# Optimization experiments

Hardware: AMD Instinct MI355X
Metric: run time of the kernel (lower is better)

## Reference

```python
import jax, jax.numpy as jnp
import numpy as np

NUM_HEADS = 4

def setup_inputs() -> dict:
    key = jax.random.key(0)
    ks = jax.random.split(key, 5)
    B, H, W, C = 4, 64, 64, 256
    x = jax.random.normal(ks[0], (B, H, W, C), dtype=jnp.float32)
    w_qkv = jax.random.normal(ks[1], (C, 3 * C), dtype=jnp.float32) * (C ** -0.5)
    b_qkv = jax.random.normal(ks[2], (3 * C,), dtype=jnp.float32) * 0.02
    w_out = jax.random.normal(ks[3], (C, C), dtype=jnp.float32) * (C ** -0.5)
    b_out = jax.random.normal(ks[4], (C,), dtype=jnp.float32) * 0.02
    return {"x": x, "w_qkv": w_qkv, "b_qkv": b_qkv, "w_out": w_out, "b_out": b_out}

def reference(x, w_qkv, b_qkv, w_out, b_out):
    B, H, W, C = x.shape
    nh = NUM_HEADS
    hd = C // nh
    scale = hd ** -0.5
    N = H * W
    # qkv projection: [B, N, 3, nh, hd]
    qkv = (x.reshape(B, N, C) @ w_qkv + b_qkv).reshape(B, N, 3, nh, hd)
    q, k, v = jnp.moveaxis(qkv, 2, 0)          # each [B, N, nh, hd]
    q = jnp.swapaxes(q, 1, 2)                  # [B, nh, N, hd]
    k = jnp.swapaxes(k, 1, 2)
    v = jnp.swapaxes(v, 1, 2)
    attn = jax.nn.softmax(jnp.einsum('bhnd,bhmd->bhnm', q * scale, k), axis=-1)
    o = jnp.einsum('bhnm,bhmd->bhnd', attn, v)  # [B, nh, N, hd]
    o = jnp.swapaxes(o, 1, 2).reshape(B, H, W, C)
    return o @ w_out + b_out
```

## Files before the change

kernel.cpp:

```cpp
#include <hip/hip_runtime.h>
#include <stdint.h>

typedef unsigned short u16;
typedef __attribute__((ext_vector_type(8))) short bf16x8;
typedef __attribute__((ext_vector_type(4))) float f32x4;

#define QSCL 0.1803368801111244f

#define GLD_LDS16(g, l) __builtin_amdgcn_global_load_lds( \
    (const __attribute__((address_space(1))) void*)(g),    \
    (__attribute__((address_space(3))) void*)(l), 16, 0, 0)

__device__ __forceinline__ u16 f2bf(float f) {
    union { uint32_t i; float f; } v; v.f = f;
    uint32_t i = v.i;
    return (u16)((i + 0x7FFFu + ((i >> 16) & 1u)) >> 16);
}
__device__ __forceinline__ uint32_t fbits(float f) {
    union { float f; uint32_t i; } v; v.f = f; return v.i;
}
__device__ __forceinline__ float bits2f(uint32_t i) {
    union { uint32_t i; float f; } v; v.i = i; return v.f;
}

__global__ __launch_bounds__(256)
void transpose_kernel(const float* __restrict__ src, u16* __restrict__ dst,
                      int R, int Ctiles) {
    __shared__ u16 T[64][68];
    const int t = threadIdx.x;
    const int rt = blockIdx.x / Ctiles;
    const int ct = blockIdx.x % Ctiles;
    const int C = Ctiles << 6;

    for (int i = 0; i < 4; i++) {
        int idx = t + 256 * i;
        int row = idx >> 4;
        int col4 = (idx & 15) << 2;
        float4 d = *(const float4*)(src + (size_t)(rt * 64 + row) * C + ct * 64 + col4);
        T[col4 + 0][row] = f2bf(d.x);
        T[col4 + 1][row] = f2bf(d.y);
        T[col4 + 2][row] = f2bf(d.z);
        T[col4 + 3][row] = f2bf(d.w);
    }
    __syncthreads();
    for (int i = 0; i < 4; i++) {
        int idx = t + 256 * i;
        int row = idx >> 4;
        int col4 = (idx & 15) << 2;
        uint2 d = *(const uint2*)&T[row][col4];
        *(uint2*)(dst + (size_t)(ct * 64 + row) * R + rt * 64 + col4) = d;
    }
}

__global__ __launch_bounds__(256)
void convert_kernel(const float* __restrict__ x, u16* __restrict__ xbf) {
    size_t i = ((size_t)blockIdx.x * 256 + threadIdx.x) * 4;
    float4 d = *(const float4*)(x + i);
    u16 e[4] = {f2bf(d.x), f2bf(d.y), f2bf(d.z), f2bf(d.w)};
    *(uint2*)(xbf + i) = *(uint2*)e;
}

__global__ __launch_bounds__(256)
void gemm_qkv_old(const float* __restrict__ X, const u16* __restrict__ Wt,
                  const float* __restrict__ Bias, u16* __restrict__ QK,
                  u16* __restrict__ Vt) {
    __shared__ __align__(16) u16 As[64][40];
    __shared__ __align__(16) u16 Bts[64][40];

    const int t = threadIdx.x;
    const int lane = t & 63;
    const int wave = t >> 6;
    const int l15 = lane & 15;
    const int l4 = lane >> 4;

    const int ntile = blockIdx.x % 12;
    const int mbase = (blockIdx.x / 12) << 6;

    f32x4 acc[4];
    for (int c = 0; c < 4; c++) acc[c] = (f32x4){0.f, 0.f, 0.f, 0.f};

    for (int kc = 0; kc < 256; kc += 32) {
        __syncthreads();
        for (int i = 0; i < 2; i++) {
            int idx = t + 256 * i;
            int row = idx >> 3;
            int col4 = (idx & 7) << 2;
            float4 d = *(const float4*)(X + (size_t)(mbase + row) * 256 + kc + col4);
            u16 e[4] = {f2bf(d.x), f2bf(d.y), f2bf(d.z), f2bf(d.w)};
            *(uint2*)&As[row][col4] = *(uint2*)e;
        }
        for (int i = 0; i < 2; i++) {
            int idx = t + 256 * i;
            int row = idx >> 3;
            int col4 = (idx & 7) << 2;
            uint2 w = *(const uint2*)(Wt + (size_t)(ntile * 64 + row) * 256 + kc + col4);
            *(uint2*)&Bts[row][col4] = w;
        }
        __syncthreads();

        bf16x8 a = *(const bf16x8*)&As[wave * 16 + l15][l4 * 8];
        for (int c = 0; c < 4; c++) {
            bf16x8 b = *(const bf16x8*)&Bts[c * 16 + l15][l4 * 8];
            acc[c] = __builtin_amdgcn_mfma_f32_16x16x32_bf16(a, b, acc[c], 0, 0, 0);
        }
    }

    if (ntile < 8) {
        const float scl = (ntile < 4) ? QSCL : 1.0f;
        for (int c = 0; c < 4; c++) {
            int colc = c * 16 + l15;
            float bv = Bias[ntile * 64 + colc];
            for (int r = 0; r < 4; r++) {
                int row = mbase + wave * 16 + l4 * 4 + r;
                QK[(size_t)row * 512 + ntile * 64 + colc] = f2bf((acc[c][r] + bv) * scl);
            }
        }
    } else {
        const int h = ntile - 8;
        for (int c = 0; c < 4; c++) {
            int d = c * 16 + l15;
            float bv = Bias[512 + h * 64 + d];
            int n = mbase + wave * 16 + l4 * 4;
            int b = n >> 12;
            int nin = n & 4095;
            u16 e[4] = {f2bf(acc[c][0] + bv), f2bf(acc[c][1] + bv),
                        f2bf(acc[c][2] + bv), f2bf(acc[c][3] + bv)};
            *(uint2*)(Vt + ((size_t)(b * 4 + h) * 64 + d) * 4096 + nin) = *(uint2*)e;
        }
    }
}

__global__ __launch_bounds__(256)
void gemm_out_old(const u16* __restrict__ Wt2, const float* __restrict__ Bias,
                  float* __restrict__ IO) {
    __shared__ __align__(16) u16 As[64][264];
    __shared__ __align__(16) u16 Wts[256][40];

    const int t = threadIdx.x;
    const int lane = t & 63;
    const int wave = t >> 6;
    const int l15 = lane & 15;
    const int l4 = lane >> 4;
    const int mbase = blockIdx.x << 6;

    for (int i = 0; i < 16; i++) {
        int idx = t + 256 * i;
        int row = idx >> 6;
        int col4 = (idx & 63) << 2;
        float4 d = *(const float4*)(IO + (size_t)(mbase + row) * 256 + col4);
        u16 e[4] = {f2bf(d.x), f2bf(d.y), f2bf(d.z), f2bf(d.w)};
        *(uint2*)&As[row][col4] = *(uint2*)e;
    }

    f32x4 acc[4][4];
    for (int nt = 0; nt < 4; nt++)
        for (int c = 0; c < 4; c++) acc[nt][c] = (f32x4){0.f, 0.f, 0.f, 0.f};

    for (int kc = 0; kc < 256; kc += 32) {
        __syncthreads();
        for (int i = 0; i < 8; i++) {
            int idx = t + 256 * i;
            int row = idx >> 3;
            int col4 = (idx & 7) << 2;
            uint2 w = *(const uint2*)(Wt2 + (size_t)row * 256 + kc + col4);
            *(uint2*)&Wts[row][col4] = w;
        }
        __syncthreads();

        bf16x8 a = *(const bf16x8*)&As[wave * 16 + l15][kc + l4 * 8];
        for (int nt = 0; nt < 4; nt++)
            for (int c = 0; c < 4; c++) {
                bf16x8 b = *(const bf16x8*)&Wts[nt * 64 + c * 16 + l15][l4 * 8];
                acc[nt][c] = __builtin_amdgcn_mfma_f32_16x16x32_bf16(a, b, acc[nt][c], 0, 0, 0);
            }
    }

    for (int nt = 0; nt < 4; nt++)
        for (int c = 0; c < 4; c++) {
            int coln = nt * 64 + c * 16 + l15;
            float bv = Bias[coln];
            for (int r = 0; r < 4; r++) {
                int row = mbase + wave * 16 + l4 * 4 + r;
                IO[(size_t)row * 256 + coln] = acc[nt][c][r] + bv;
            }
        }
}

__global__ __launch_bounds__(256)
void gemm_qkv_new(const u16* __restrict__ Abf, const u16* __restrict__ Bt,
                  const float* __restrict__ Bias, u16* __restrict__ QK,
                  u16* __restrict__ Vt) {
    __shared__ __align__(16) u16 As[128 * 32];
    __shared__ __align__(16) u16 Bs[128 * 32];

    const int t = threadIdx.x;
    const int lane = t & 63;
    const int wave = t >> 6;
    const int l15 = lane & 15;
    const int l4 = lane >> 4;
    const int wm = wave >> 1, wn = wave & 1;

    const int mb = blockIdx.x / 6;
    const int nb = blockIdx.x % 6;

    const u16* gA[2]; const u16* gB[2]; int ldsoff[2];
    #pragma unroll
    for (int i = 0; i < 2; i++) {
        int chunk = i * 256 + t;
        int row = chunk >> 2;
        int sch = (chunk & 3) ^ (row & 3);
        gA[i] = Abf + (size_t)(mb * 128 + row) * 256 + sch * 8;
        gB[i] = Bt + (size_t)(nb * 128 + row) * 256 + sch * 8;
        ldsoff[i] = (i * 256 + wave * 64) * 8;
    }
    int offA[4], offB[4];
    #pragma unroll
    for (int c = 0; c < 4; c++) {
        offA[c] = (wm * 64 + c * 16 + l15) * 32 + ((l4 ^ (l15 & 3)) * 8);
        offB[c] = (wn * 64 + c * 16 + l15) * 32 + ((l4 ^ (l15 & 3)) * 8);
    }

    f32x4 acc[4][4];
    #pragma unroll
    for (int cm = 0; cm < 4; cm++)
        for (int cn = 0; cn < 4; cn++) acc[cm][cn] = (f32x4){0.f, 0.f, 0.f, 0.f};

    for (int kc = 0; kc < 256; kc += 32) {
        __syncthreads();
        #pragma unroll
        for (int i = 0; i < 2; i++) {
            GLD_LDS16(gA[i] + kc, As + ldsoff[i]);
            GLD_LDS16(gB[i] + kc, Bs + ldsoff[i]);
        }
        __syncthreads();

        bf16x8 a[4], b[4];
        #pragma unroll
        for (int c = 0; c < 4; c++) {
            a[c] = *(const bf16x8*)(As + offA[c]);
            b[c] = *(const bf16x8*)(Bs + offB[c]);
        }
        #pragma unroll
        for (int cm = 0; cm < 4; cm++)
            #pragma unroll
            for (int cn = 0; cn < 4; cn++)
                acc[cm][cn] = __builtin_amdgcn_mfma_f32_16x16x32_bf16(
                    a[cm], b[cn], acc[cm][cn], 0, 0, 0);
    }

    #pragma unroll
    for (int cn = 0; cn < 4; cn++) {
        int n = nb * 128 + wn * 64 + cn * 16 + l15;
        float bv = Bias[n];
        int slice = n >> 6;
        if (slice < 4) {
            #pragma unroll
            for (int cm = 0; cm < 4; cm++) {
                int m0 = mb * 128 + wm * 64 + cm * 16 + l4 * 4;
                for (int r = 0; r < 4; r++)
                    QK[(size_t)(m0 + r) * 512 + n] = f2bf((acc[cm][cn][r] + bv) * QSCL);
            }
        } else if (slice < 8) {
            #pragma unroll
            for (int cm = 0; cm < 4; cm++) {
                int m0 = mb * 128 + wm * 64 + cm * 16 + l4 * 4;
                for (int r = 0; r < 4; r++)
                    QK[(size_t)(m0 + r) * 512 + n] = f2bf(acc[cm][cn][r] + bv);
            }
        } else {
            int h = slice - 8;
            int d = n & 63;
            #pragma unroll
            for (int cm = 0; cm < 4; cm++) {
                int m0 = mb * 128 + wm * 64 + cm * 16 + l4 * 4;
                int b_ = m0 >> 12;
                int nin = m0 & 4095;
                u16 e[4] = {f2bf(acc[cm][cn][0] + bv), f2bf(acc[cm][cn][1] + bv),
                            f2bf(acc[cm][cn][2] + bv), f2bf(acc[cm][cn][3] + bv)};
                *(uint2*)(Vt + ((size_t)(b_ * 4 + h) * 64 + d) * 4096 + nin) = *(uint2*)e;
            }
        }
    }
}

__global__ __launch_bounds__(256)
void gemm_out_new(const u16* __restrict__ Obf, const u16* __restrict__ Wt2,
                  const float* __restrict__ Bias, float* __restrict__ out) {
    __shared__ __align__(16) u16 As[128 * 32];
    __shared__ __align__(16) u16 Bs[128 * 32];

    const int t = threadIdx.x;
    const int lane = t & 63;
    const int wave = t >> 6;
    const int l15 = lane & 15;
    const int l4 = lane >> 4;
    const int wm = wave >> 1, wn = wave & 1;

    const int mb = blockIdx.x >> 1;
    const int nb = blockIdx.x & 1;

    const u16* gA[2]; const u16* gB[2]; int ldsoff[2];
    #pragma unroll
    for (int i = 0; i < 2; i++) {
        int chunk = i * 256 + t;
        int row = chunk >> 2;
        int sch = (chunk & 3) ^ (row & 3);
        gA[i] = Obf + (size_t)(mb * 128 + row) * 256 + sch * 8;
        gB[i] = Wt2 + (size_t)(nb * 128 + row) * 256 + sch * 8;
        ldsoff[i] = (i * 256 + wave * 64) * 8;
    }
    int offA[4], offB[4];
    #pragma unroll
    for (int c = 0; c < 4; c++) {
        offA[c] = (wm * 64 + c * 16 + l15) * 32 + ((l4 ^ (l15 & 3)) * 8);
        offB[c] = (wn * 64 + c * 16 + l15) * 32 + ((l4 ^ (l15 & 3)) * 8);
    }

    f32x4 acc[4][4];
    #pragma unroll
    for (int cm = 0; cm < 4; cm++)
        for (int cn = 0; cn < 4; cn++) acc[cm][cn] = (f32x4){0.f, 0.f, 0.f, 0.f};

    for (int kc = 0; kc < 256; kc += 32) {
        __syncthreads();
        #pragma unroll
        for (int i = 0; i < 2; i++) {
            GLD_LDS16(gA[i] + kc, As + ldsoff[i]);
            GLD_LDS16(gB[i] + kc, Bs + ldsoff[i]);
        }
        __syncthreads();

        bf16x8 a[4], b[4];
        #pragma unroll
        for (int c = 0; c < 4; c++) {
            a[c] = *(const bf16x8*)(As + offA[c]);
            b[c] = *(const bf16x8*)(Bs + offB[c]);
        }
        #pragma unroll
        for (int cm = 0; cm < 4; cm++)
            #pragma unroll
            for (int cn = 0; cn < 4; cn++)
                acc[cm][cn] = __builtin_amdgcn_mfma_f32_16x16x32_bf16(
                    a[cm], b[cn], acc[cm][cn], 0, 0, 0);
    }

    #pragma unroll
    for (int cn = 0; cn < 4; cn++) {
        int n = nb * 128 + wn * 64 + cn * 16 + l15;
        float bv = Bias[n];
        #pragma unroll
        for (int cm = 0; cm < 4; cm++) {
            int m0 = mb * 128 + wm * 64 + cm * 16 + l4 * 4;
            for (int r = 0; r < 4; r++)
                out[(size_t)(m0 + r) * 256 + n] = acc[cm][cn][r] + bv;
        }
    }
}

__global__ __launch_bounds__(256, 4)
void attn_kernel(const u16* __restrict__ QK, const u16* __restrict__ Vt,
                 float* __restrict__ Of, u16* __restrict__ Obf, int writebf,
                 int bhmask, int bhbits) {
    __shared__ __align__(16) u16 Kt[2][64][64];
    __shared__ __align__(16) u16 Vts[2][64][64];
    __shared__ __align__(16) u16 Ps[4][16][64];

    const int t = threadIdx.x;
    const int lane = t & 63;
    const int wave = t >> 6;
    const int l15 = lane & 15;
    const int l4 = lane >> 4;

    const int bh = blockIdx.x & bhmask;
    const int qb = blockIdx.x >> bhbits;
    const int b = bh >> 2;
    const int h = bh & 3;

    const size_t qkbase = (size_t)b * 4096 * 512;
    const size_t vtbase = (size_t)bh * 64 * 4096;
    const int q0 = qb * 64 + wave * 16;

    const u16* gk[2]; const u16* gv[2]; u16* lk[2]; u16* lv[2];
    #pragma unroll
    for (int i = 0; i < 2; i++) {
        int chunk = i * 256 + t;
        int row = chunk >> 3;
        int sch = (chunk & 7) ^ (row & 7);
        gk[i] = QK + qkbase + (size_t)row * 512 + 256 + h * 64 + sch * 8;
        gv[i] = Vt + vtbase + (size_t)row * 4096 + sch * 8;
        int cbase = (i * 256 + wave * 64) * 8;
        lk[i] = &Kt[0][0][0] + cbase;
        lv[i] = &Vts[0][0][0] + cbase;
    }
    int koff[4][2];
    #pragma unroll
    for (int c = 0; c < 4; c++) {
        int row = c * 16 + l15;
        int sw = row & 7;
        koff[c][0] = row * 64 + ((0 + l4) ^ sw) * 8;
        koff[c][1] = row * 64 + ((4 + l4) ^ sw) * 8;
    }
    u16* psbase = &Ps[wave][l15][0];
    int offw[4], offr[2];
    #pragma unroll
    for (int c = 0; c < 4; c++)
        offw[c] = (((2 * c + (l4 >> 1)) ^ (l15 & 7)) << 3) + ((l4 & 1) << 2);
    #pragma unroll
    for (int kk = 0; kk < 2; kk++)
        offr[kk] = (((4 * kk + l4) ^ (l15 & 7)) << 3);

    bf16x8 qf[2];
    #pragma unroll
    for (int kk = 0; kk < 2; kk++)
        qf[kk] = *(const bf16x8*)(QK + qkbase
            + (size_t)(q0 + l15) * 512 + h * 64 + kk * 32 + l4 * 8);

    f32x4 Oacc[4];
    #pragma unroll
    for (int c = 0; c < 4; c++) Oacc[c] = (f32x4){0.f, 0.f, 0.f, 0.f};
    float lsum = 0.f;

    auto stageKV = [&](int buf, int jn) {
        #pragma unroll
        for (int i = 0; i < 2; i++) {
            GLD_LDS16(gk[i] + (size_t)jn * 32768, lk[i] + buf * 4096);
            GLD_LDS16(gv[i] + jn * 64,            lv[i] + buf * 4096);
        }
    };

    auto body = [&](int par, int jn) {
        __syncthreads();
        stageKV(par ^ 1, jn);

        const u16* kb = &Kt[0][0][0] + par * 4096;
        const u16* vb = &Vts[0][0][0] + par * 4096;

        f32x4 s[4];
        #pragma unroll
        for (int c = 0; c < 4; c++) s[c] = (f32x4){0.f, 0.f, 0.f, 0.f};
        #pragma unroll
        for (int c = 0; c < 4; c++) {
            bf16x8 k0 = *(const bf16x8*)(kb + koff[c][0]);
            bf16x8 k1 = *(const bf16x8*)(kb + koff[c][1]);
            s[c] = __builtin_amdgcn_mfma_f32_16x16x32_bf16(k0, qf[0], s[c], 0, 0, 0);
            s[c] = __builtin_amdgcn_mfma_f32_16x16x32_bf16(k1, qf[1], s[c], 0, 0, 0);
        }

        float ls = 0.f;
        #pragma unroll
        for (int c = 0; c < 4; c++) {
            f32x4 sv = s[c];
            uint32_t u0 = fbits(__builtin_exp2f(sv[0]));
            uint32_t u1 = fbits(__builtin_exp2f(sv[1]));
            uint32_t u2 = fbits(__builtin_exp2f(sv[2]));
            uint32_t u3 = fbits(__builtin_exp2f(sv[3]));
            float t0 = bits2f(u0 & 0xFFFF0000u);
            float t1 = bits2f(u1 & 0xFFFF0000u);
            float t2 = bits2f(u2 & 0xFFFF0000u);
            float t3 = bits2f(u3 & 0xFFFF0000u);
            ls += (t0 + t1) + (t2 + t3);
            uint2 pk;
            pk.x = __builtin_amdgcn_perm(u1, u0, 0x07060302u);
            pk.y = __builtin_amdgcn_perm(u3, u2, 0x07060302u);
            *(uint2*)(psbase + offw[c]) = pk;
        }
        lsum += ls;

        __threadfence_block();

        bf16x8 bp[2];
        #pragma unroll
        for (int kk = 0; kk < 2; kk++)
            bp[kk] = *(const bf16x8*)(psbase + offr[kk]);

        #pragma unroll
        for (int c = 0; c < 4; c++) {
            bf16x8 v0 = *(const bf16x8*)(vb + koff[c][0]);
            bf16x8 v1 = *(const bf16x8*)(vb + koff[c][1]);
            Oacc[c] = __builtin_amdgcn_mfma_f32_16x16x32_bf16(v0, bp[0], Oacc[c], 0, 0, 0);
            Oacc[c] = __builtin_amdgcn_mfma_f32_16x16x32_bf16(v1, bp[1], Oacc[c], 0, 0, 0);
        }
    };

    stageKV(0, 0);
    for (int jt = 0; jt < 64; jt += 2) {
        body(0, jt + 1);
        body(1, (jt + 2) & 63);
    }

    float l = lsum;
    l += __shfl_xor(l, 16);
    l += __shfl_xor(l, 32);
    float inv = 1.f / l;
    size_t row = (size_t)b * 4096 + q0 + l15;
    if (writebf) {
        #pragma unroll
        for (int c = 0; c < 4; c++) {
            f32x4 o = Oacc[c] * inv;
            u16 e[4] = {f2bf(o[0]), f2bf(o[1]), f2bf(o[2]), f2bf(o[3])};
            *(uint2*)(Obf + row * 256 + h * 64 + c * 16 + l4 * 4) = *(uint2*)e;
        }
    } else {
        #pragma unroll
        for (int c = 0; c < 4; c++) {
            f32x4 o = Oacc[c] * inv;
            *(f32x4*)(Of + row * 256 + h * 64 + c * 16 + l4 * 4) = o;
        }
    }
}

extern "C" void kernel_launch(void* const* d_in, const int* in_sizes, int n_in,
                              void* d_out, int out_size, void* d_ws, size_t ws_size,
                              hipStream_t stream) {
    const float* x     = (const float*)d_in[0];
    const float* w_qkv = (const float*)d_in[1];
    const float* b_qkv = (const float*)d_in[2];
    const float* w_out = (const float*)d_in[3];
    const float* b_out = (const float*)d_in[4];
    float* out = (float*)d_out;

    char* ws = (char*)d_ws;
    u16* Wt  = (u16*)ws;
    u16* Wt2 = (u16*)(ws + 393216);
    u16* QK  = (u16*)(ws + 524288);
    u16* Vt  = (u16*)(ws + 524288 + 16777216);
    u16* XO  = (u16*)(ws + 524288 + 16777216 + 8388608);
    const size_t NEED_NEW = 524288 + 16777216 + 8388608 + 8388608;

    transpose_kernel<<<dim3(48), dim3(256), 0, stream>>>(w_qkv, Wt, 256, 12);
    transpose_kernel<<<dim3(16), dim3(256), 0, stream>>>(w_out, Wt2, 256, 4);

    if (ws_size >= NEED_NEW) {
        convert_kernel<<<dim3(4096), dim3(256), 0, stream>>>(x, XO);
        gemm_qkv_new<<<dim3(768), dim3(256), 0, stream>>>(XO, Wt, b_qkv, QK, Vt);
        attn_kernel<<<dim3(1024), dim3(256), 0, stream>>>(
            QK, Vt, out, XO, 1, 15, 4);
        gemm_out_new<<<dim3(256), dim3(256), 0, stream>>>(XO, Wt2, b_out, out);
    } else {
        gemm_qkv_old<<<dim3(3072), dim3(256), 0, stream>>>(x, Wt, b_qkv, QK, Vt);
        attn_kernel<<<dim3(1024), dim3(256), 0, stream>>>(
            QK, Vt, out, (u16*)nullptr, 0, 15, 4);
        gemm_out_old<<<dim3(256), dim3(256), 0, stream>>>(Wt2, b_out, out);
    }
}
```

Measured before the change: 224.5 us.

## Use raw exp2, hardware bf16 pack, zero-init MFMA and improved LDS swizzle

The attention inner loop now uses the raw hardware exp2 builtin instead of the libm-style exp2f. It packs probabilities with v_cvt_pk_bf16_f32 instead of truncating through bit masks and perm, and feeds a zero accumulator straight into the first MFMA instead of zeroing a separate accumulator. The K/V LDS XOR swizzle also mixes in row>>3 to change bank mapping on the MFMA reads. The row sum now uses unrounded fp32 probabilities while P is rounded to nearest bf16, so the normalisation no longer matches the truncated values exactly.

Result: faster. 213.2 us (-5.0%).

```diff
diff --git a/kernel.cpp b/kernel.cpp
--- a/kernel.cpp
+++ b/kernel.cpp
@@ -10,17 +10,17 @@
 #define GLD_LDS16(g, l) __builtin_amdgcn_global_load_lds( \
     (const __attribute__((address_space(1))) void*)(g),    \
     (__attribute__((address_space(3))) void*)(l), 16, 0, 0)
+
+#if __has_builtin(__builtin_amdgcn_exp2f)
+#define EXP2(x) __builtin_amdgcn_exp2f(x)
+#else
+#define EXP2(x) __builtin_exp2f(x)
+#endif
 
 __device__ __forceinline__ u16 f2bf(float f) {
     union { uint32_t i; float f; } v; v.f = f;
     uint32_t i = v.i;
     return (u16)((i + 0x7FFFu + ((i >> 16) & 1u)) >> 16);
-}
-__device__ __forceinline__ uint32_t fbits(float f) {
-    union { float f; uint32_t i; } v; v.f = f; return v.i;
-}
-__device__ __forceinline__ float bits2f(uint32_t i) {
-    union { uint32_t i; float f; } v; v.i = i; return v.f;
 }
 
 __global__ __launch_bounds__(256)
@@ -385,7 +385,7 @@
     for (int i = 0; i < 2; i++) {
         int chunk = i * 256 + t;
         int row = chunk >> 3;
-        int sch = (chunk & 7) ^ (row & 7);
+        int sch = (chunk & 7) ^ ((row ^ (row >> 3)) & 7);
         gk[i] = QK + qkbase + (size_t)row * 512 + 256 + h * 64 + sch * 8;
         gv[i] = Vt + vtbase + (size_t)row * 4096 + sch * 8;
         int cbase = (i * 256 + wave * 64) * 8;
@@ -396,7 +396,7 @@
     #pragma unroll
     for (int c = 0; c < 4; c++) {
         int row = c * 16 + l15;
-        int sw = row & 7;
+        int sw = (row ^ (row >> 3)) & 7;
         koff[c][0] = row * 64 + ((0 + l4) ^ sw) * 8;
         koff[c][1] = row * 64 + ((4 + l4) ^ sw) * 8;
     }
@@ -415,9 +415,11 @@
         qf[kk] = *(const bf16x8*)(QK + qkbase
             + (size_t)(q0 + l15) * 512 + h * 64 + kk * 32 + l4 * 8);
 
+    const f32x4 z4 = (f32x4){0.f, 0.f, 0.f, 0.f};
+
     f32x4 Oacc[4];
     #pragma unroll
-    for (int c = 0; c < 4; c++) Oacc[c] = (f32x4){0.f, 0.f, 0.f, 0.f};
+    for (int c = 0; c < 4; c++) Oacc[c] = z4;
     float lsum = 0.f;
 
     auto stageKV = [&](int buf, int jn) {
@@ -437,12 +439,10 @@
 
         f32x4 s[4];
         #pragma unroll
-        for (int c = 0; c < 4; c++) s[c] = (f32x4){0.f, 0.f, 0.f, 0.f};
-        #pragma unroll
         for (int c = 0; c < 4; c++) {
             bf16x8 k0 = *(const bf16x8*)(kb + koff[c][0]);
             bf16x8 k1 = *(const bf16x8*)(kb + koff[c][1]);
-            s[c] = __builtin_amdgcn_mfma_f32_16x16x32_bf16(k0, qf[0], s[c], 0, 0, 0);
+            s[c] = __builtin_amdgcn_mfma_f32_16x16x32_bf16(k0, qf[0], z4, 0, 0, 0);
             s[c] = __builtin_amdgcn_mfma_f32_16x16x32_bf16(k1, qf[1], s[c], 0, 0, 0);
         }
 
@@ -450,18 +450,14 @@
         #pragma unroll
         for (int c = 0; c < 4; c++) {
             f32x4 sv = s[c];
-            uint32_t u0 = fbits(__builtin_exp2f(sv[0]));
-            uint32_t u1 = fbits(__builtin_exp2f(sv[1]));
-            uint32_t u2 = fbits(__builtin_exp2f(sv[2]));
-            uint32_t u3 = fbits(__builtin_exp2f(sv[3]));
-            float t0 = bits2f(u0 & 0xFFFF0000u);
-            float t1 = bits2f(u1 & 0xFFFF0000u);
-            float t2 = bits2f(u2 & 0xFFFF0000u);
-            float t3 = bits2f(u3 & 0xFFFF0000u);
-            ls += (t0 + t1) + (t2 + t3);
+            float p0 = EXP2(sv[0]);
+            float p1 = EXP2(sv[1]);
+            float p2 = EXP2(sv[2]);
+            float p3 = EXP2(sv[3]);
+            ls += (p0 + p1) + (p2 + p3);
             uint2 pk;
-            pk.x = __builtin_amdgcn_perm(u1, u0, 0x07060302u);
-            pk.y = __builtin_amdgcn_perm(u3, u2, 0x07060302u);
+            asm("v_cvt_pk_bf16_f32 %0, %1, %2" : "=v"(pk.x) : "v"(p0), "v"(p1));
+            asm("v_cvt_pk_bf16_f32 %0, %1, %2" : "=v"(pk.y) : "v"(p2), "v"(p3));
             *(uint2*)(psbase + offw[c]) = pk;
         }
         lsum += ls;
```
